# Kernel optimization log

Hardware: AMD Instinct MI355X
Metric: run time of the kernel (lower is better)

Reference implementation:

```python
import jax, jax.numpy as jnp
import numpy as np

B, L, H, E = 8, 1024, 8, 64
S = 1024
T = 1.0


def setup_inputs() -> dict:
    key = jax.random.key(0)
    kq, kk, kv = jax.random.split(key, 3)
    q = jax.random.normal(kq, (B, L, H, E), dtype=jnp.float32)
    k = jax.random.normal(kk, (B, S, H, E), dtype=jnp.float32)
    v = jax.random.normal(kv, (B, S, H, E), dtype=jnp.float32)
    attn_mask = jnp.zeros((1,), dtype=bool)  # unused by the module
    return {"q": q, "k": k, "v": v, "attn_mask": attn_mask}


def reference(q, k, v, attn_mask):
    # q: [B,L,H,E], k/v: [B,S,H,E]; attn_mask unused (matches torch source)
    Bq, Lq, Hq, Eq = q.shape
    xq = jnp.transpose(q, (0, 2, 3, 1))  # [B,H,E,L]
    xk = jnp.transpose(k, (0, 2, 3, 1))  # [B,H,E,S]
    xv = jnp.transpose(v, (0, 2, 3, 1))  # [B,H,E,S]
    qf = jnp.fft.rfft(xq, axis=-1, norm="ortho")  # [B,H,E,Lf]
    kf = jnp.fft.rfft(xk, axis=-1, norm="ortho")  # [B,H,E,Sf]
    vf = jnp.fft.rfft(xv, axis=-1, norm="ortho")  # [B,H,E,Sf]
    # complex cross-frequency scores, contracted over head dim E
    scores = jnp.einsum("bhex,bhey->bhxy", qf, jnp.conj(kf)) / jnp.sqrt(
        jnp.float32(Eq)
    )  # [B,H,Lf,Sf] complex
    # magnitude softmax -> real weights, promoted back to complex (zero imag)
    attn = jax.nn.softmax(jnp.abs(scores) / jnp.float32(T), axis=-1)
    attn = attn.astype(scores.dtype)
    outf = jnp.einsum("bhxy,bhey->bhex", attn, vf)  # [B,H,E,Lf] complex
    out = jnp.fft.irfft(outf, n=Lq, axis=-1, norm="ortho")  # [B,H,E,L] real
    return jnp.transpose(out, (0, 3, 1, 2))  # [B,L,H,E]
```

## Files before the change

kernel.cpp:

```cpp
#include <hip/hip_runtime.h>
#include <hip/hip_fp16.h>
#include <math.h>

#define BATCH 8
#define LSEQ  1024
#define NH    8
#define EDIM  64
#define LF    513
#define NBH   64
#define YP    576

typedef _Float16 f16;
typedef _Float16 f16x8 __attribute__((ext_vector_type(8)));
typedef float    f32x4 __attribute__((ext_vector_type(4)));
typedef unsigned int u32x4 __attribute__((ext_vector_type(4)));

__device__ __forceinline__ void fft_stages(float2* src, float2* dst,
                                           const float2* __restrict__ tw,
                                           int t, float sign) {
  int s = 1, ls = 0, n = 1024;
  #pragma unroll
  for (int st = 0; st < 10; st++) {
    int m = n >> 1;
    int p = t >> ls;
    int q = t & (s - 1);
    float2 a = src[q + s * p];
    float2 b = src[q + s * p + s * m];
    float2 w = tw[p * s];
    float wr = w.x, wi = sign * w.y;
    float2 r0 = make_float2(a.x + b.x, a.y + b.y);
    float2 d  = make_float2(a.x - b.x, a.y - b.y);
    float2 r1 = make_float2(d.x * wr - d.y * wi, d.x * wi + d.y * wr);
    dst[q + s * 2 * p]     = r0;
    dst[q + s * 2 * p + s] = r1;
    __syncthreads();
    float2* tmp = src; src = dst; dst = tmp;
    n >>= 1; s <<= 1; ls++;
  }
}

__global__ __launch_bounds__(512) void rfft_pack_kernel(
    const float* __restrict__ q, const float* __restrict__ k, const float* __restrict__ v,
    f16* __restrict__ qf, f16* __restrict__ kf, f16* __restrict__ vfT) {
  __shared__ float2 b0[1024];
  __shared__ float2 b1[1024];
  __shared__ float2 tw[512];
  const int t = threadIdx.x;
  const int epair = blockIdx.x;
  const int bh = blockIdx.y;
  const int tensor = blockIdx.z;
  const int b = bh >> 3, h = bh & 7;
  const int e = epair * 2;
  const float* src = (tensor == 0) ? q : ((tensor == 1) ? k : v);

  float sv, cv;
  __sincosf(6.2831853071795864769f * (float)t * (1.0f / 1024.0f), &sv, &cv);
  tw[t] = make_float2(cv, sv);
  #pragma unroll
  for (int i = 0; i < 2; i++) {
    int l = t + i * 512;
    const float* p = src + (((size_t)b * LSEQ + l) * NH + h) * EDIM + e;
    b0[l] = make_float2(p[0], p[1]);
  }
  __syncthreads();
  fft_stages(b0, b1, tw, t, -1.0f);
  #pragma unroll
  for (int i = 0; i < 2; i++) {
    int kk = t + i * 512;
    if (kk <= 512) {
      float2 z  = b0[kk];
      float2 zn = b0[(1024 - kk) & 1023];
      const float sc = 0.03125f * 0.5f;
      float ar = sc * (z.x + zn.x);
      float ai = sc * (z.y - zn.y);
      float br = sc * (z.y + zn.y);
      float bi = sc * (zn.x - z.x);
      if (tensor < 2) {
        f16* dst = (tensor == 0) ? qf : kf;
        union { f16 h[4]; uint2 u; } pk;
        pk.h[0] = (f16)ar; pk.h[1] = (f16)ai; pk.h[2] = (f16)br; pk.h[3] = (f16)bi;
        *(uint2*)(dst + ((size_t)bh * YP + kk) * 128 + e * 2) = pk.u;
      } else {
        size_t base = (size_t)bh * 128 + e * 2;
        vfT[(base + 0) * YP + kk] = (f16)ar;
        vfT[(base + 1) * YP + kk] = (f16)ai;
        vfT[(base + 2) * YP + kk] = (f16)br;
        vfT[(base + 3) * YP + kk] = (f16)bi;
      }
    }
  }
  if (tensor == 2 && t < 63) {
    int kk = 513 + t;
    size_t base = (size_t)bh * 128 + e * 2;
    #pragma unroll
    for (int j = 0; j < 4; j++) vfT[(base + j) * YP + kk] = (f16)0.0f;
  }
}

__device__ __forceinline__ int pmidx(int row, int y) {
  return row * YP + (y ^ ((row & 7) << 3));
}

__global__ __launch_bounds__(256, 4) void fused_attn_kernel(
    const f16* __restrict__ qf, const f16* __restrict__ kf,
    const f16* __restrict__ vfT, float* __restrict__ of) {
  __shared__ f16 pm[32 * YP];
  __shared__ float winv_s[32];
  const int tid = threadIdx.x;
  const int w = tid >> 6, l = tid & 63, lr = l & 15, lg = l >> 4;
  const int bh = blockIdx.y, x0 = blockIdx.x * 32;
  const int xsub = w & 1, yhalf = w >> 1;

  for (int i = tid; i < 2048; i += 256) {
    int row = i >> 6, yo = i & 63;
    if (yo) pm[pmidx(row, 512 + yo)] = (f16)0.0f;
  }

  const f16* qb = qf + ((size_t)bh * YP + x0 + xsub * 16 + lr) * 128 + lg * 8;
  f16x8 aq[4], aqs[4];
  #pragma unroll
  for (int c4 = 0; c4 < 4; c4++) {
    aq[c4] = *(const f16x8*)(qb + c4 * 32);
    u32x4 tt = *(const u32x4*)&aq[c4];
    u32x4 ss;
    #pragma unroll
    for (int d = 0; d < 4; d++)
      ss[d] = ((tt[d] >> 16) | (tt[d] << 16)) ^ 0x80000000u;
    aqs[c4] = *(const f16x8*)&ss;
  }

  const int ntile = yhalf ? 15 : 18;
  const f16* kb = kf + ((size_t)bh * YP + yhalf * 288 + lr) * 128 + lg * 8;
  for (int t = 0; t < ntile; t++) {
    f16x8 bk[4];
    #pragma unroll
    for (int c4 = 0; c4 < 4; c4++)
      bk[c4] = *(const f16x8*)(kb + (size_t)(t * 16) * 128 + c4 * 32);
    f32x4 rr = {0.f,0.f,0.f,0.f}, ri = {0.f,0.f,0.f,0.f};
    #pragma unroll
    for (int c4 = 0; c4 < 4; c4++) {
      rr = __builtin_amdgcn_mfma_f32_16x16x32_f16(aq[c4],  bk[c4], rr, 0, 0, 0);
      ri = __builtin_amdgcn_mfma_f32_16x16x32_f16(aqs[c4], bk[c4], ri, 0, 0, 0);
    }
    int y = yhalf * 288 + t * 16 + lr;
    if (y <= 512) {
      int rowb = xsub * 16 + lg * 4;
      #pragma unroll
      for (int i = 0; i < 4; i++)
        pm[pmidx(rowb + i, y)] = (f16)(0.125f * sqrtf(rr[i]*rr[i] + ri[i]*ri[i]));
    }
  }
  __syncthreads();

  #pragma unroll 1
  for (int r = 0; r < 8; r++) {
    const int row = w * 8 + r;
    float mx = 0.0f;
    #pragma unroll
    for (int ps = 0; ps < 4; ps++) {
      __half2 hv = *(const __half2*)&pm[pmidx(row, 2 * (l + 64 * ps))];
      float2 f = __half22float2(hv);
      mx = fmaxf(mx, fmaxf(f.x, f.y));
    }
    if (l < 32) {
      __half2 hv = *(const __half2*)&pm[pmidx(row, 512 + 2 * l)];
      float2 f = __half22float2(hv);
      mx = fmaxf(mx, fmaxf(f.x, f.y));
    }
    #pragma unroll
    for (int o = 32; o > 0; o >>= 1) mx = fmaxf(mx, __shfl_xor(mx, o));

    float s = 0.0f;
    #pragma unroll
    for (int ps = 0; ps < 4; ps++) {
      int y = 2 * (l + 64 * ps);
      __half2 hv = *(const __half2*)&pm[pmidx(row, y)];
      float2 f = __half22float2(hv);
      float p0 = __expf(f.x - mx), p1 = __expf(f.y - mx);
      s += p0 + p1;
      *(__half2*)&pm[pmidx(row, y)] = __floats2half2_rn(p0, p1);
    }
    if (l < 32) {
      int y = 512 + 2 * l;
      __half2 hv = *(const __half2*)&pm[pmidx(row, y)];
      float2 f = __half22float2(hv);
      float p0 = (y <= 512) ? __expf(f.x - mx) : 0.0f;
      s += p0;
      *(__half2*)&pm[pmidx(row, y)] = __floats2half2_rn(p0, 0.0f);
    }
    #pragma unroll
    for (int o = 32; o > 0; o >>= 1) s += __shfl_xor(s, o);
    if (l == 0) winv_s[row] = 1.0f / s;
  }
  __syncthreads();

  const int ch = (w >> 1) * 64;
  f32x4 acc[4];
  #pragma unroll
  for (int nt = 0; nt < 4; nt++) acc[nt] = (f32x4){0.f,0.f,0.f,0.f};
  const f16* vb = vfT + ((size_t)bh * 128 + ch + lr) * YP + lg * 8;
  for (int kc = 0; kc < 18; kc++) {
    f16x8 a = *(const f16x8*)&pm[pmidx(xsub * 16 + lr, kc * 32 + lg * 8)];
    #pragma unroll
    for (int nt = 0; nt < 4; nt++) {
      f16x8 b = *(const f16x8*)(vb + (size_t)(nt * 16) * YP + kc * 32);
      acc[nt] = __builtin_amdgcn_mfma_f32_16x16x32_f16(a, b, acc[nt], 0, 0, 0);
    }
  }
  #pragma unroll
  for (int i = 0; i < 4; i++) {
    int xl = xsub * 16 + lg * 4 + i;
    int x = x0 + xl;
    if (x < LF) {
      float wv = winv_s[xl];
      #pragma unroll
      for (int nt = 0; nt < 4; nt++)
        of[((size_t)bh * LF + x) * 128 + ch + nt * 16 + lr] = acc[nt][i] * wv;
    }
  }
}

__global__ __launch_bounds__(512) void irfft_kernel(
    const float* __restrict__ of, float* __restrict__ out) {
  __shared__ float2 b0[1024];
  __shared__ float2 b1[1024];
  __shared__ float2 tw[512];
  const int t = threadIdx.x;
  const int epair = blockIdx.x;
  const int bh = blockIdx.y;
  const int b = bh >> 3, h = bh & 7;
  const int e = epair * 2;

  float sv, cv;
  __sincosf(6.2831853071795864769f * (float)t * (1.0f / 1024.0f), &sv, &cv);
  tw[t] = make_float2(cv, sv);
  #pragma unroll
  for (int i = 0; i < 2; i++) {
    int kk = t + i * 512;
    if (kk <= 512) {
      const float* p = of + ((size_t)bh * LF + kk) * 128 + e * 2;
      float far = p[0], fai = p[1], fbr = p[2], fbi = p[3];
      b0[kk] = make_float2(far - fbi, fai + fbr);
      if (kk >= 1 && kk <= 511) {
        b0[1024 - kk] = make_float2(far + fbi, fbr - fai);
      }
    }
  }
  __syncthreads();
  fft_stages(b0, b1, tw, t, +1.0f);
  #pragma unroll
  for (int i = 0; i < 2; i++) {
    int l = t + i * 512;
    float2 z = b0[l];
    float* o = out + (((size_t)b * LSEQ + l) * NH + h) * EDIM + e;
    o[0] = 0.03125f * z.x;
    o[1] = 0.03125f * z.y;
  }
}

extern "C" void kernel_launch(void* const* d_in, const int* in_sizes, int n_in,
                              void* d_out, int out_size, void* d_ws, size_t ws_size,
                              hipStream_t stream) {
  const float* q = (const float*)d_in[0];
  const float* k = (const float*)d_in[1];
  const float* v = (const float*)d_in[2];
  float* out = (float*)d_out;
  char* ws = (char*)d_ws;

  f16*   qf  = (f16*)(ws);
  f16*   kf  = (f16*)(ws + 9437184);
  f16*   vfT = (f16*)(ws + 18874368);
  float* of  = (float*)(ws + 28311552);

  rfft_pack_kernel<<<dim3(32, NBH, 3), 512, 0, stream>>>(q, k, v, qf, kf, vfT);
  fused_attn_kernel<<<dim3(17, NBH), 256, 0, stream>>>(qf, kf, vfT, of);
  irfft_kernel<<<dim3(32, NBH), 512, 0, stream>>>(of, out);
}
```

Measured before the change: 309.0 us.

## Use radix-4 FFT on two column pairs per block and double-buffer MFMA loads

The forward and inverse FFT kernels switch from a 10-stage radix-2 shared-memory FFT to a 5-stage radix-4 FFT. Each block now processes two e-pairs at once, with vectorized float4 global loads and stores, which halves the block count and the number of barriers per transform. Separately, the attention kernel double-buffers the K-tile loads in the score loop and the V-tile loads in the PV loop so global loads overlap MFMA work. The cost is more shared memory per FFT block and more live registers in the attention kernel, which could lower occupancy.

```diff
diff --git a/kernel.cpp b/kernel.cpp
--- a/kernel.cpp
+++ b/kernel.cpp
@@ -15,85 +15,111 @@
 typedef float    f32x4 __attribute__((ext_vector_type(4)));
 typedef unsigned int u32x4 __attribute__((ext_vector_type(4)));
 
-__device__ __forceinline__ void fft_stages(float2* src, float2* dst,
-                                           const float2* __restrict__ tw,
-                                           int t, float sign) {
-  int s = 1, ls = 0, n = 1024;
-  #pragma unroll
-  for (int st = 0; st < 10; st++) {
-    int m = n >> 1;
-    int p = t >> ls;
-    int q = t & (s - 1);
-    float2 a = src[q + s * p];
-    float2 b = src[q + s * p + s * m];
-    float2 w = tw[p * s];
-    float wr = w.x, wi = sign * w.y;
-    float2 r0 = make_float2(a.x + b.x, a.y + b.y);
-    float2 d  = make_float2(a.x - b.x, a.y - b.y);
-    float2 r1 = make_float2(d.x * wr - d.y * wi, d.x * wi + d.y * wr);
-    dst[q + s * 2 * p]     = r0;
-    dst[q + s * 2 * p + s] = r1;
-    __syncthreads();
-    float2* tmp = src; src = dst; dst = tmp;
-    n >>= 1; s <<= 1; ls++;
-  }
+__device__ __forceinline__ float2 cadd(float2 a, float2 b){return make_float2(a.x+b.x, a.y+b.y);}
+__device__ __forceinline__ float2 csub(float2 a, float2 b){return make_float2(a.x-b.x, a.y-b.y);}
+__device__ __forceinline__ float2 cmuls(float2 w, float2 y, float sign){
+  float wr = w.x, wi = sign * w.y;
+  return make_float2(y.x*wr - y.y*wi, y.x*wi + y.y*wr);
+}
+
+template<int ST>
+__device__ __forceinline__ void r4stage(const float2* S, float2* D,
+                                        const float2* __restrict__ tw,
+                                        int bt, float sign) {
+  const int s = 1 << (2*ST);
+  const int q = bt & (s - 1);
+  const int j1 = bt - q;
+  float2 a0 = S[bt], a1 = S[bt+256], a2 = S[bt+512], a3 = S[bt+768];
+  float2 b0 = cadd(a0,a2), b1 = csub(a0,a2);
+  float2 b2 = cadd(a1,a3), b3 = csub(a1,a3);
+  float2 y0 = cadd(b0,b2), y2 = csub(b0,b2);
+  float2 ib3 = make_float2(-sign*b3.y, sign*b3.x);
+  float2 y1 = cadd(b1, ib3), y3 = csub(b1, ib3);
+  const int wb = 4*bt - 3*q;
+  D[wb]       = y0;
+  D[wb +   s] = cmuls(tw[j1],   y1, sign);
+  D[wb + 2*s] = cmuls(tw[2*j1], y2, sign);
+  D[wb + 3*s] = cmuls(tw[3*j1], y3, sign);
+}
+
+__device__ __forceinline__ void fft1024x2_r4(float2* fb0, float2* fb1,
+                                             const float2* __restrict__ tw,
+                                             int t, float sign) {
+  const int off = (t >> 8) << 10;
+  const int bt  = t & 255;
+  r4stage<0>(fb0+off, fb1+off, tw, bt, sign); __syncthreads();
+  r4stage<1>(fb1+off, fb0+off, tw, bt, sign); __syncthreads();
+  r4stage<2>(fb0+off, fb1+off, tw, bt, sign); __syncthreads();
+  r4stage<3>(fb1+off, fb0+off, tw, bt, sign); __syncthreads();
+  r4stage<4>(fb0+off, fb1+off, tw, bt, sign); __syncthreads();
 }
 
 __global__ __launch_bounds__(512) void rfft_pack_kernel(
     const float* __restrict__ q, const float* __restrict__ k, const float* __restrict__ v,
     f16* __restrict__ qf, f16* __restrict__ kf, f16* __restrict__ vfT) {
-  __shared__ float2 b0[1024];
-  __shared__ float2 b1[1024];
-  __shared__ float2 tw[512];
+  __shared__ float2 fb0[2048];
+  __shared__ float2 fb1[2048];
+  __shared__ float2 tw[768];
   const int t = threadIdx.x;
-  const int epair = blockIdx.x;
+  const int equad = blockIdx.x;
   const int bh = blockIdx.y;
   const int tensor = blockIdx.z;
   const int b = bh >> 3, h = bh & 7;
-  const int e = epair * 2;
+  const int e0 = equad * 4;
   const float* src = (tensor == 0) ? q : ((tensor == 1) ? k : v);
 
-  float sv, cv;
-  __sincosf(6.2831853071795864769f * (float)t * (1.0f / 1024.0f), &sv, &cv);
-  tw[t] = make_float2(cv, sv);
+  for (int i = t; i < 768; i += 512) {
+    float sv, cv;
+    __sincosf(6.2831853071795864769f * (float)i * (1.0f / 1024.0f), &sv, &cv);
+    tw[i] = make_float2(cv, sv);
+  }
   #pragma unroll
   for (int i = 0; i < 2; i++) {
     int l = t + i * 512;
-    const float* p = src + (((size_t)b * LSEQ + l) * NH + h) * EDIM + e;
-    b0[l] = make_float2(p[0], p[1]);
+    float4 vv = *(const float4*)(src + (((size_t)b * LSEQ + l) * NH + h) * EDIM + e0);
+    fb0[l]        = make_float2(vv.x, vv.y);
+    fb0[1024 + l] = make_float2(vv.z, vv.w);
   }
   __syncthreads();
-  fft_stages(b0, b1, tw, t, -1.0f);
+  fft1024x2_r4(fb0, fb1, tw, t, -1.0f);
+
   #pragma unroll
   for (int i = 0; i < 2; i++) {
     int kk = t + i * 512;
     if (kk <= 512) {
-      float2 z  = b0[kk];
-      float2 zn = b0[(1024 - kk) & 1023];
-      const float sc = 0.03125f * 0.5f;
-      float ar = sc * (z.x + zn.x);
-      float ai = sc * (z.y - zn.y);
-      float br = sc * (z.y + zn.y);
-      float bi = sc * (zn.x - z.x);
+      const float sc = 0.015625f;
       if (tensor < 2) {
+        union { f16 hh[8]; u32x4 u; } pk;
+        #pragma unroll
+        for (int f = 0; f < 2; f++) {
+          float2 z  = fb1[(f << 10) + kk];
+          float2 zn = fb1[(f << 10) + ((1024 - kk) & 1023)];
+          pk.hh[f*4+0] = (f16)(sc * (z.x + zn.x));
+          pk.hh[f*4+1] = (f16)(sc * (z.y - zn.y));
+          pk.hh[f*4+2] = (f16)(sc * (z.y + zn.y));
+          pk.hh[f*4+3] = (f16)(sc * (zn.x - z.x));
+        }
         f16* dst = (tensor == 0) ? qf : kf;
-        union { f16 h[4]; uint2 u; } pk;
-        pk.h[0] = (f16)ar; pk.h[1] = (f16)ai; pk.h[2] = (f16)br; pk.h[3] = (f16)bi;
-        *(uint2*)(dst + ((size_t)bh * YP + kk) * 128 + e * 2) = pk.u;
+        *(u32x4*)(dst + ((size_t)bh * YP + kk) * 128 + e0 * 2) = pk.u;
       } else {
-        size_t base = (size_t)bh * 128 + e * 2;
-        vfT[(base + 0) * YP + kk] = (f16)ar;
-        vfT[(base + 1) * YP + kk] = (f16)ai;
-        vfT[(base + 2) * YP + kk] = (f16)br;
-        vfT[(base + 3) * YP + kk] = (f16)bi;
+        #pragma unroll
+        for (int f = 0; f < 2; f++) {
+          float2 z  = fb1[(f << 10) + kk];
+          float2 zn = fb1[(f << 10) + ((1024 - kk) & 1023)];
+          size_t base = (size_t)bh * 128 + e0 * 2 + f * 4;
+          vfT[(base + 0) * YP + kk] = (f16)(sc * (z.x + zn.x));
+          vfT[(base + 1) * YP + kk] = (f16)(sc * (z.y - zn.y));
+          vfT[(base + 2) * YP + kk] = (f16)(sc * (z.y + zn.y));
+          vfT[(base + 3) * YP + kk] = (f16)(sc * (zn.x - z.x));
+        }
       }
     }
   }
   if (tensor == 2 && t < 63) {
     int kk = 513 + t;
-    size_t base = (size_t)bh * 128 + e * 2;
-    #pragma unroll
-    for (int j = 0; j < 4; j++) vfT[(base + j) * YP + kk] = (f16)0.0f;
+    #pragma unroll
+    for (int j = 0; j < 8; j++)
+      vfT[((size_t)bh * 128 + e0 * 2 + j) * YP + kk] = (f16)0.0f;
   }
 }
 
@@ -131,25 +157,44 @@
 
   const int ntile = yhalf ? 15 : 18;
   const f16* kb = kf + ((size_t)bh * YP + yhalf * 288 + lr) * 128 + lg * 8;
-  for (int t = 0; t < ntile; t++) {
-    f16x8 bk[4];
-    #pragma unroll
-    for (int c4 = 0; c4 < 4; c4++)
-      bk[c4] = *(const f16x8*)(kb + (size_t)(t * 16) * 128 + c4 * 32);
-    f32x4 rr = {0.f,0.f,0.f,0.f}, ri = {0.f,0.f,0.f,0.f};
-    #pragma unroll
-    for (int c4 = 0; c4 < 4; c4++) {
-      rr = __builtin_amdgcn_mfma_f32_16x16x32_f16(aq[c4],  bk[c4], rr, 0, 0, 0);
-      ri = __builtin_amdgcn_mfma_f32_16x16x32_f16(aqs[c4], bk[c4], ri, 0, 0, 0);
-    }
-    int y = yhalf * 288 + t * 16 + lr;
-    if (y <= 512) {
-      int rowb = xsub * 16 + lg * 4;
-      #pragma unroll
-      for (int i = 0; i < 4; i++)
-        pm[pmidx(rowb + i, y)] = (f16)(0.125f * sqrtf(rr[i]*rr[i] + ri[i]*ri[i]));
-    }
-  }
+
+  f16x8 kA[4], kB[4];
+  #pragma unroll
+  for (int c4 = 0; c4 < 4; c4++) kA[c4] = *(const f16x8*)(kb + c4 * 32);
+
+#define PROCA(KR, TT) {                                                        \
+    f32x4 rr = {0.f,0.f,0.f,0.f}, ri = {0.f,0.f,0.f,0.f};                      \
+    _Pragma("unroll")                                                          \
+    for (int c4 = 0; c4 < 4; c4++) {                                           \
+      rr = __builtin_amdgcn_mfma_f32_16x16x32_f16(aq[c4],  KR[c4], rr, 0,0,0); \
+      ri = __builtin_amdgcn_mfma_f32_16x16x32_f16(aqs[c4], KR[c4], ri, 0,0,0); \
+    }                                                                          \
+    int y = yhalf * 288 + (TT) * 16 + lr;                                      \
+    if (y <= 512) {                                                            \
+      int rowb = xsub * 16 + lg * 4;                                           \
+      _Pragma("unroll")                                                        \
+      for (int i = 0; i < 4; i++)                                              \
+        pm[pmidx(rowb + i, y)] = (f16)(0.125f * sqrtf(rr[i]*rr[i] + ri[i]*ri[i])); \
+    }                                                                          \
+  }
+
+  for (int t = 0; t < ntile; t += 2) {
+    if (t + 1 < ntile) {
+      const f16* kp = kb + (size_t)(t + 1) * 2048;
+      #pragma unroll
+      for (int c4 = 0; c4 < 4; c4++) kB[c4] = *(const f16x8*)(kp + c4 * 32);
+    }
+    PROCA(kA, t)
+    if (t + 1 < ntile) {
+      if (t + 2 < ntile) {
+        const f16* kp = kb + (size_t)(t + 2) * 2048;
+        #pragma unroll
+        for (int c4 = 0; c4 < 4; c4++) kA[c4] = *(const f16x8*)(kp + c4 * 32);
+      }
+      PROCA(kB, t + 1)
+    }
+  }
+#undef PROCA
   __syncthreads();
 
   #pragma unroll 1
@@ -199,12 +244,31 @@
   #pragma unroll
   for (int nt = 0; nt < 4; nt++) acc[nt] = (f32x4){0.f,0.f,0.f,0.f};
   const f16* vb = vfT + ((size_t)bh * 128 + ch + lr) * YP + lg * 8;
-  for (int kc = 0; kc < 18; kc++) {
-    f16x8 a = *(const f16x8*)&pm[pmidx(xsub * 16 + lr, kc * 32 + lg * 8)];
-    #pragma unroll
-    for (int nt = 0; nt < 4; nt++) {
-      f16x8 b = *(const f16x8*)(vb + (size_t)(nt * 16) * YP + kc * 32);
-      acc[nt] = __builtin_amdgcn_mfma_f32_16x16x32_f16(a, b, acc[nt], 0, 0, 0);
+
+  f16x8 vA[4], vB[4];
+  #pragma unroll
+  for (int nt = 0; nt < 4; nt++) vA[nt] = *(const f16x8*)(vb + (size_t)(nt * 16) * YP);
+
+  for (int kc = 0; kc < 18; kc += 2) {
+    #pragma unroll
+    for (int nt = 0; nt < 4; nt++)
+      vB[nt] = *(const f16x8*)(vb + (size_t)(nt * 16) * YP + (kc + 1) * 32);
+    {
+      f16x8 a = *(const f16x8*)&pm[pmidx(xsub * 16 + lr, kc * 32 + lg * 8)];
+      #pragma unroll
+      for (int nt = 0; nt < 4; nt++)
+        acc[nt] = __builtin_amdgcn_mfma_f32_16x16x32_f16(a, vA[nt], acc[nt], 0, 0, 0);
+    }
+    if (kc + 2 < 18) {
+      #pragma unroll
+      for (int nt = 0; nt < 4; nt++)
+        vA[nt] = *(const f16x8*)(vb + (size_t)(nt * 16) * YP + (kc + 2) * 32);
+    }
+    {
+      f16x8 a = *(const f16x8*)&pm[pmidx(xsub * 16 + lr, (kc + 1) * 32 + lg * 8)];
+      #pragma unroll
+      for (int nt = 0; nt < 4; nt++)
+        acc[nt] = __builtin_amdgcn_mfma_f32_16x16x32_f16(a, vB[nt], acc[nt], 0, 0, 0);
     }
   }
   #pragma unroll
@@ -222,39 +286,44 @@
 
 __global__ __launch_bounds__(512) void irfft_kernel(
     const float* __restrict__ of, float* __restrict__ out) {
-  __shared__ float2 b0[1024];
-  __shared__ float2 b1[1024];
-  __shared__ float2 tw[512];
+  __shared__ float2 fb0[2048];
+  __shared__ float2 fb1[2048];
+  __shared__ float2 tw[768];
   const int t = threadIdx.x;
-  const int epair = blockIdx.x;
+  const int equad = blockIdx.x;
   const int bh = blockIdx.y;
   const int b = bh >> 3, h = bh & 7;
-  const int e = epair * 2;
-
-  float sv, cv;
-  __sincosf(6.2831853071795864769f * (float)t * (1.0f / 1024.0f), &sv, &cv);
-  tw[t] = make_float2(cv, sv);
+  const int e0 = equad * 4;
+
+  for (int i = t; i < 768; i += 512) {
+    float sv, cv;
+    __sincosf(6.2831853071795864769f * (float)i * (1.0f / 1024.0f), &sv, &cv);
+    tw[i] = make_float2(cv, sv);
+  }
   #pragma unroll
   for (int i = 0; i < 2; i++) {
     int kk = t + i * 512;
     if (kk <= 512) {
-      const float* p = of + ((size_t)bh * LF + kk) * 128 + e * 2;
-      float far = p[0], fai = p[1], fbr = p[2], fbi = p[3];
-      b0[kk] = make_float2(far - fbi, fai + fbr);
+      const float* pr = of + ((size_t)bh * LF + kk) * 128 + e0 * 2;
+      float4 r0 = *(const float4*)pr;
+      float4 r1 = *(const float4*)(pr + 4);
+      fb0[kk]        = make_float2(r0.x - r0.w, r0.y + r0.z);
+      fb0[1024 + kk] = make_float2(r1.x - r1.w, r1.y + r1.z);
       if (kk >= 1 && kk <= 511) {
-        b0[1024 - kk] = make_float2(far + fbi, fbr - fai);
+        fb0[1024 - kk]        = make_float2(r0.x + r0.w, r0.z - r0.y);
+        fb0[1024 + 1024 - kk] = make_float2(r1.x + r1.w, r1.z - r1.y);
       }
     }
   }
   __syncthreads();
-  fft_stages(b0, b1, tw, t, +1.0f);
+  fft1024x2_r4(fb0, fb1, tw, t, +1.0f);
   #pragma unroll
   for (int i = 0; i < 2; i++) {
     int l = t + i * 512;
-    float2 z = b0[l];
-    float* o = out + (((size_t)b * LSEQ + l) * NH + h) * EDIM + e;
-    o[0] = 0.03125f * z.x;
-    o[1] = 0.03125f * z.y;
+    float2 z0 = fb1[l], z1 = fb1[1024 + l];
+    float4 o = make_float4(0.03125f * z0.x, 0.03125f * z0.y,
+                           0.03125f * z1.x, 0.03125f * z1.y);
+    *(float4*)(out + (((size_t)b * LSEQ + l) * NH + h) * EDIM + e0) = o;
   }
 }
 
@@ -272,7 +341,7 @@
   f16*   vfT = (f16*)(ws + 18874368);
   float* of  = (float*)(ws + 28311552);
 
-  rfft_pack_kernel<<<dim3(32, NBH, 3), 512, 0, stream>>>(q, k, v, qf, kf, vfT);
+  rfft_pack_kernel<<<dim3(16, NBH, 3), 512, 0, stream>>>(q, k, v, qf, kf, vfT);
   fused_attn_kernel<<<dim3(17, NBH), 256, 0, stream>>>(qf, kf, vfT, of);
-  irfft_kernel<<<dim3(32, NBH), 512, 0, stream>>>(of, out);
-}
+  irfft_kernel<<<dim3(16, NBH), 512, 0, stream>>>(of, out);
+}
```

Result: faster. 262.5 us (-15.1%).
